# Kernel tuning notes

Measured on AMD Instinct MI355X. Metric: run time of the kernel, lower is better.

## Reference

```python
import jax, jax.numpy as jnp
import numpy as np

D_IN = 2048
D_OUT = 2048
LN_EPS = 1e-5


def setup_inputs() -> dict:
    key = jax.random.key(0)
    kx, kw, kb = jax.random.split(key, 3)
    x = jax.random.normal(kx, (8, 2048, D_IN), dtype=jnp.float32)
    # LayerNorm affine params (torch defaults: ones / zeros)
    gamma = jnp.ones((D_IN,), dtype=jnp.float32)
    beta = jnp.zeros((D_IN,), dtype=jnp.float32)
    # weight = rand(out,in)*0.001, bias = rand(out)*0.001, alpha = ones(out)
    weight = jax.random.uniform(kw, (D_OUT, D_IN), dtype=jnp.float32) * 0.001
    bias = jax.random.uniform(kb, (D_OUT,), dtype=jnp.float32) * 0.001
    alpha = jnp.ones((D_OUT,), dtype=jnp.float32)
    return {"x": x, "gamma": gamma, "beta": beta, "weight": weight,
            "bias": bias, "alpha": alpha}


def reference(x, gamma, beta, weight, bias, alpha):
    # LayerNorm over last dim (biased variance, eps=1e-5, affine)
    mu = jnp.mean(x, axis=-1, keepdims=True)
    var = jnp.mean(jnp.square(x - mu), axis=-1, keepdims=True)
    xn = (x - mu) * jax.lax.rsqrt(var + LN_EPS) * gamma + beta
    # Binarize activations: hard sign
    a = jnp.sign(xn)
    # Binarize weights: mean-center per output row, clip, sign (STE in fwd == sign)
    centered = weight - jnp.mean(weight, axis=1, keepdims=True)  # [O, I]
    signed_w = jnp.sign(centered)
    # Linear + bias, then per-output-channel alpha scale
    out = jnp.einsum('bsi,oi->bso', a, signed_w) + bias
    return out * alpha
```

## Files before the change

### kernel.cpp

```cpp
#include <hip/hip_runtime.h>

#define DIN 2048
#define WPR 64
#define QPR 32
#define GPR 16
#define RPB 8
#define LN_EPS 1e-5f

#define GLOBAL_AS __attribute__((address_space(1)))
#define LDS_AS    __attribute__((address_space(3)))

typedef unsigned long long u64;
typedef int   i32x4  __attribute__((ext_vector_type(4)));
typedef int   i32x8  __attribute__((ext_vector_type(8)));
typedef float f32x16 __attribute__((ext_vector_type(16)));

__device__ inline float wave_sum(float v) {
    #pragma unroll
    for (int off = 32; off; off >>= 1) v += __shfl_down(v, off, 64);
    return v;
}


__global__ __launch_bounds__(256) void expand_kernel(const float* __restrict__ x,
                                                     const float* __restrict__ gamma,
                                                     const float* __restrict__ beta,
                                                     const float* __restrict__ w,
                                                     char* __restrict__ Aexp,
                                                     char* __restrict__ Bexp,
                                                     int Mblocks) {
    const int t = threadIdx.x;
    const int wid = t >> 6, lane = t & 63;
    __shared__ float red[4][2 * RPB];
    __shared__ __align__(16) unsigned stg[RPB * 256];

    const bool isA = (int)blockIdx.x < Mblocks;
    const int r0 = (isA ? (int)blockIdx.x : ((int)blockIdx.x - Mblocks)) * RPB;
    const float* src = isA ? x : w;

    float gg[8], bb[8];
    if (isA) {
        float4 g0 = ((const float4*)gamma)[t * 2];
        float4 g1 = ((const float4*)gamma)[t * 2 + 1];
        float4 b0 = ((const float4*)beta)[t * 2];
        float4 b1 = ((const float4*)beta)[t * 2 + 1];
        gg[0]=g0.x; gg[1]=g0.y; gg[2]=g0.z; gg[3]=g0.w;
        gg[4]=g1.x; gg[5]=g1.y; gg[6]=g1.z; gg[7]=g1.w;
        bb[0]=b0.x; bb[1]=b0.y; bb[2]=b0.z; bb[3]=b0.w;
        bb[4]=b1.x; bb[5]=b1.y; bb[6]=b1.z; bb[7]=b1.w;
    }

    float vv[RPB][8];
    #pragma unroll
    for (int rr = 0; rr < RPB; ++rr) {
        const float* xr = src + (size_t)(r0 + rr) * DIN;
        float4 v0 = ((const float4*)xr)[t * 2];
        float4 v1 = ((const float4*)xr)[t * 2 + 1];
        vv[rr][0]=v0.x; vv[rr][1]=v0.y; vv[rr][2]=v0.z; vv[rr][3]=v0.w;
        vv[rr][4]=v1.x; vv[rr][5]=v1.y; vv[rr][6]=v1.z; vv[rr][7]=v1.w;
    }

    #pragma unroll
    for (int rr = 0; rr < RPB; ++rr) {
        float s = 0.f, ss = 0.f;
        #pragma unroll
        for (int j = 0; j < 8; ++j) s += vv[rr][j];
        if (isA) {
            #pragma unroll
            for (int j = 0; j < 8; ++j) ss += vv[rr][j] * vv[rr][j];
        }
        s = wave_sum(s);
        if (isA) ss = wave_sum(ss);
        if (lane == 0) { red[wid][rr * 2] = s; red[wid][rr * 2 + 1] = ss; }
    }
    __syncthreads();

    #pragma unroll
    for (int rr = 0; rr < RPB; ++rr) {
        float tot = red[0][rr*2] + red[1][rr*2] + red[2][rr*2] + red[3][rr*2];
        float mu  = tot * (1.f / DIN);
        unsigned word = 0;
        if (isA) {
            float tots = red[0][rr*2+1] + red[1][rr*2+1] + red[2][rr*2+1] + red[3][rr*2+1];
            float var  = tots * (1.f / DIN) - mu * mu;
            float rs   = rsqrtf(var + LN_EPS);
            #pragma unroll
            for (int j = 0; j < 8; ++j) {
                float xn = (vv[rr][j] - mu) * rs * gg[j] + bb[j];
                word |= (xn < 0.f ? 0xAu : 0x2u) << (4 * j);
            }
        } else {
            #pragma unroll
            for (int j = 0; j < 8; ++j)
                word |= ((vv[rr][j] - mu) < 0.f ? 0xAu : 0x2u) << (4 * j);
        }
        stg[rr * 256 + (((t >> 2) ^ rr) << 2) + (t & 3)] = word;
    }
    __syncthreads();

    char* dstbase = isA ? Aexp : Bexp;
    const int bm  = r0 >> 8;
    const int rt  = (r0 >> 5) & 7;
    const int ri0 = r0 & 31;
    #pragma unroll
    for (int i2 = 0; i2 < 2; ++i2) {
        const int u  = i2 * 256 + t;
        const int sc = u >> 5;
        const int kt = (u >> 4) & 1, hb = (u >> 3) & 1, ri = u & 7;
        const int g  = sc * 4 + kt * 2 + hb;
        uint4 v = *(const uint4*)&stg[ri * 256 + ((g ^ ri) << 2)];
        const size_t doff = (((size_t)(bm * 16 + sc)) * 8 + rt) * 2048 + kt * 1024 +
                            (ri0 + ri + 32 * hb) * 16;
        *(uint4*)(dstbase + doff) = v;
    }
}

__global__ __launch_bounds__(256, 3) void fp4gemm_kernel(const char* __restrict__ Aexp,
                                                         const char* __restrict__ Bexp,
                                                         const float* __restrict__ bias,
                                                         const float* __restrict__ alpha,
                                                         float* __restrict__ out,
                                                         int ldc, int nBmX) {
    const int t = threadIdx.x;
    const int wv = t >> 6, lane = t & 63;
    const int xcd = blockIdx.x & 7;
    const int loc = blockIdx.x >> 3;
    const int bm = xcd * nBmX + (loc % nBmX);
    const int bn = loc / nBmX;
    const int wr = wv >> 1, wc = wv & 1;

    const char* gA = Aexp + (size_t)(bm >> 1) * 262144 + (size_t)(bm & 1) * 8192 + lane * 16;
    const char* gB = Bexp + (size_t)(bn >> 1) * 262144 + (size_t)(bn & 1) * 8192 + lane * 16;

#define LOADF(S, AF, BF)                                                        \
    {                                                                           \
        _Pragma("unroll")                                                       \
        for (int kt = 0; kt < 2; ++kt) {                                        \
            _Pragma("unroll")                                                   \
            for (int i = 0; i < 2; ++i)                                         \
                AF[kt][i] = *(const i32x4*)(gA + (size_t)(S) * 16384 +          \
                                            (wr * 2 + i) * 2048 + kt * 1024);   \
            _Pragma("unroll")                                                   \
            for (int j = 0; j < 2; ++j)                                         \
                BF[kt][j] = *(const i32x4*)(gB + (size_t)(S) * 16384 +          \
                                            (wc * 2 + j) * 2048 + kt * 1024);   \
        }                                                                       \
    }

#define COMPF(AF, BF)                                                           \
    {                                                                           \
        _Pragma("unroll")                                                       \
        for (int kt = 0; kt < 2; ++kt) {                                        \
            i32x8 aa[2], bb2[2];                                                \
            _Pragma("unroll")                                                   \
            for (int i = 0; i < 2; ++i) {                                       \
                aa[i][0]=AF[kt][i][0]; aa[i][1]=AF[kt][i][1];                   \
                aa[i][2]=AF[kt][i][2]; aa[i][3]=AF[kt][i][3];                   \
                aa[i][4]=AF[kt][i][0]; aa[i][5]=AF[kt][i][1];                   \
                aa[i][6]=AF[kt][i][2]; aa[i][7]=AF[kt][i][3];                   \
                bb2[i][0]=BF[kt][i][0]; bb2[i][1]=BF[kt][i][1];                 \
                bb2[i][2]=BF[kt][i][2]; bb2[i][3]=BF[kt][i][3];                 \
                bb2[i][4]=BF[kt][i][0]; bb2[i][5]=BF[kt][i][1];                 \
                bb2[i][6]=BF[kt][i][2]; bb2[i][7]=BF[kt][i][3];                 \
            }                                                                   \
            __builtin_amdgcn_s_setprio(1);                                      \
            _Pragma("unroll")                                                   \
            for (int i = 0; i < 2; ++i)                                         \
                _Pragma("unroll")                                               \
                for (int j = 0; j < 2; ++j)                                     \
                    acc[i][j] = __builtin_amdgcn_mfma_scale_f32_32x32x64_f8f6f4(\
                        aa[i], bb2[j], acc[i][j], 4, 4,                         \
                        0, 0x7F7F7F7F, 0, 0x7F7F7F7F);                          \
            __builtin_amdgcn_s_setprio(0);                                      \
        }                                                                       \
    }

    f32x16 acc[2][2];
    #pragma unroll
    for (int i = 0; i < 2; ++i)
        #pragma unroll
        for (int j = 0; j < 2; ++j)
            #pragma unroll
            for (int e = 0; e < 16; ++e) acc[i][j][e] = 0.f;

    i32x4 af0[2][2], bf0[2][2], af1[2][2], bf1[2][2];

    LOADF(0, af0, bf0)
    #pragma unroll 1
    for (int s = 0; s < 14; s += 2) {
        LOADF(s + 1, af1, bf1)
        COMPF(af0, bf0)
        LOADF(s + 2, af0, bf0)
        COMPF(af1, bf1)
    }
    LOADF(15, af1, bf1)
    COMPF(af0, bf0)
    COMPF(af1, bf1)
#undef LOADF
#undef COMPF

    const int cl = lane & 31;
    const int rb = 4 * (lane >> 5);
    #pragma unroll
    for (int i = 0; i < 2; ++i) {
        #pragma unroll
        for (int j = 0; j < 2; ++j) {
            const int col = bn * 128 + wc * 64 + j * 32 + cl;
            const float bi = bias[col], al = alpha[col];
            const int row0 = bm * 128 + wr * 64 + i * 32 + rb;
            #pragma unroll
            for (int reg = 0; reg < 16; ++reg) {
                const int row = row0 + (reg & 3) + 8 * (reg >> 2);
                __builtin_nontemporal_store((acc[i][j][reg] + bi) * al,
                                            &out[(size_t)row * ldc + col]);
            }
        }
    }
}

__global__ __launch_bounds__(256) void w_pack_kernel(const float* __restrict__ w,
                                                     unsigned* __restrict__ wpk) {
    const int row = blockIdx.x;
    const int t = threadIdx.x;
    const float* wr = w + (size_t)row * DIN;
    float4 v0 = ((const float4*)wr)[t * 2];
    float4 v1 = ((const float4*)wr)[t * 2 + 1];
    float s = v0.x + v0.y + v0.z + v0.w + v1.x + v1.y + v1.z + v1.w;

    __shared__ float red[4];
    float wsum = wave_sum(s);
    int wid = t >> 6, lane = t & 63;
    if (lane == 0) red[wid] = wsum;
    __syncthreads();
    float mu = (red[0] + red[1] + red[2] + red[3]) * (1.f / DIN);

    float vv[8] = {v0.x, v0.y, v0.z, v0.w, v1.x, v1.y, v1.z, v1.w};
    unsigned byte = 0;
    #pragma unroll
    for (int j = 0; j < 8; ++j)
        byte |= ((vv[j] - mu) < 0.f ? 1u : 0u) << j;

    __shared__ unsigned char bytes[256];
    bytes[t] = (unsigned char)byte;
    __syncthreads();
    if (t < 64) {
        unsigned wd = (unsigned)bytes[t * 4] | ((unsigned)bytes[t * 4 + 1] << 8) |
                      ((unsigned)bytes[t * 4 + 2] << 16) | ((unsigned)bytes[t * 4 + 3] << 24);
        wpk[(size_t)row * WPR + t] = wd;
    }
}

__global__ __launch_bounds__(256) void ln_pack_kernel(const float* __restrict__ x,
                                                      const float* __restrict__ gamma,
                                                      const float* __restrict__ beta,
                                                      unsigned* __restrict__ apk) {
    const int row = blockIdx.x;
    const int t = threadIdx.x;
    const float* xr = x + (size_t)row * DIN;
    float4 v0 = ((const float4*)xr)[t * 2];
    float4 v1 = ((const float4*)xr)[t * 2 + 1];
    float s  = v0.x + v0.y + v0.z + v0.w + v1.x + v1.y + v1.z + v1.w;
    float ss = v0.x * v0.x + v0.y * v0.y + v0.z * v0.z + v0.w * v0.w +
               v1.x * v1.x + v1.y * v1.y + v1.z * v1.z + v1.w * v1.w;

    __shared__ float red[8];
    float wsum = wave_sum(s), wssum = wave_sum(ss);
    int wid = t >> 6, lane = t & 63;
    if (lane == 0) { red[wid] = wsum; red[4 + wid] = wssum; }
    __syncthreads();
    float tot  = red[0] + red[1] + red[2] + red[3];
    float tots = red[4] + red[5] + red[6] + red[7];
    float mu  = tot * (1.f / DIN);
    float var = tots * (1.f / DIN) - mu * mu;
    float rs  = rsqrtf(var + LN_EPS);

    float4 g0 = ((const float4*)gamma)[t * 2];
    float4 g1 = ((const float4*)gamma)[t * 2 + 1];
    float4 b0 = ((const float4*)beta)[t * 2];
    float4 b1 = ((const float4*)beta)[t * 2 + 1];
    float vv[8] = {v0.x, v0.y, v0.z, v0.w, v1.x, v1.y, v1.z, v1.w};
    float gg[8] = {g0.x, g0.y, g0.z, g0.w, g1.x, g1.y, g1.z, g1.w};
    float bb[8] = {b0.x, b0.y, b0.z, b0.w, b1.x, b1.y, b1.z, b1.w};
    unsigned byte = 0;
    #pragma unroll
    for (int j = 0; j < 8; ++j) {
        float xn = (vv[j] - mu) * rs * gg[j] + bb[j];
        byte |= (xn < 0.f ? 1u : 0u) << j;
    }

    __shared__ unsigned char bytes[256];
    bytes[t] = (unsigned char)byte;
    __syncthreads();
    if (t < 64) {
        unsigned wd = (unsigned)bytes[t * 4] | ((unsigned)bytes[t * 4 + 1] << 8) |
                      ((unsigned)bytes[t * 4 + 2] << 16) | ((unsigned)bytes[t * 4 + 3] << 24);
        apk[(size_t)row * WPR + t] = wd;
    }
}

__global__ __launch_bounds__(256) void bingemm_kernel(const u64* __restrict__ A,
                                                      const u64* __restrict__ B,
                                                      const float* __restrict__ bias,
                                                      const float* __restrict__ alpha,
                                                      float* __restrict__ out) {
    __shared__ u64 S[2 * 128 * QPR];
    uint4* Sg = (uint4*)S;
    const int t = threadIdx.x;
    const int bn = blockIdx.x, bm = blockIdx.y;

    const uint4* Ag = (const uint4*)(A + (size_t)bm * 128 * QPR);
    #pragma unroll
    for (int i = 0; i < 8; ++i) {
        int id = t + i * 256;
        int row = id >> 4, g = id & 15;
        Sg[(row << 4) + (g ^ (row & 15))] = Ag[id];
    }
    const uint4* Bg = (const uint4*)(B + (size_t)bn * 128 * QPR);
    #pragma unroll
    for (int i = 0; i < 8; ++i) {
        int id = t + i * 256;
        int row = id >> 4, g = id & 15;
        Sg[2048 + (row << 4) + (g ^ (row & 15))] = Bg[id];
    }
    __syncthreads();

    const int tr = t >> 4;
    const int tc = t & 15;
    const ulonglong2* Sq = (const ulonglong2*)S;
    const int abase = tr * GPR;
    const int bbase = 2048 + tc * GPR;

    int acc[8][8] = {};
    u64 a0[8][2], b0[8][2], a1[8][2], b1[8][2];

#define LOADK(KK, AR, BR)                                            \
    {                                                                \
        const int ka = abase + ((KK) ^ tr);                          \
        const int kb = bbase + ((KK) ^ tc);                          \
        _Pragma("unroll")                                            \
        for (int r = 0; r < 8; ++r) {                                \
            ulonglong2 v = Sq[ka + r * 256];                         \
            AR[r][0] = v.x; AR[r][1] = v.y;                          \
        }                                                            \
        _Pragma("unroll")                                            \
        for (int c2 = 0; c2 < 8; ++c2) {                             \
            ulonglong2 v = Sq[kb + c2 * 256];                        \
            BR[c2][0] = v.x; BR[c2][1] = v.y;                        \
        }                                                            \
    }

#define COMPK(AR, BR)                                                \
    {                                                                \
        _Pragma("unroll")                                            \
        for (int r = 0; r < 8; ++r) {                                \
            _Pragma("unroll")                                        \
            for (int c2 = 0; c2 < 8; ++c2) {                         \
                acc[r][c2] += __popcll(AR[r][0] ^ BR[c2][0]);        \
                acc[r][c2] += __popcll(AR[r][1] ^ BR[c2][1]);        \
            }                                                        \
        }                                                            \
    }

    LOADK(0, a0, b0);
    #pragma unroll 1
    for (int kk = 0; kk < 14; kk += 2) {
        LOADK(kk + 1, a1, b1);
        COMPK(a0, b0);
        LOADK(kk + 2, a0, b0);
        COMPK(a1, b1);
    }
    LOADK(15, a1, b1);
    COMPK(a0, b0);
    COMPK(a1, b1);
#undef LOADK
#undef COMPK

    float bi[8], al[8];
    #pragma unroll
    for (int c2 = 0; c2 < 8; ++c2) {
        int col = bn * 128 + tc + 16 * c2;
        bi[c2] = bias[col];
        al[c2] = alpha[col];
    }
    #pragma unroll
    for (int r = 0; r < 8; ++r) {
        const size_t row = (size_t)bm * 128 + tr + 16 * r;
        float* op = out + row * 2048 + bn * 128 + tc;
        #pragma unroll
        for (int c2 = 0; c2 < 8; ++c2)
            op[16 * c2] = ((float)(DIN - 2 * acc[r][c2]) + bi[c2]) * al[c2];
    }
}

extern "C" void kernel_launch(void* const* d_in, const int* in_sizes, int n_in,
                              void* d_out, int out_size, void* d_ws, size_t ws_size,
                              hipStream_t stream) {
    const float* x     = (const float*)d_in[0];
    const float* gamma = (const float*)d_in[1];
    const float* beta  = (const float*)d_in[2];
    const float* w     = (const float*)d_in[3];
    const float* bias  = (const float*)d_in[4];
    const float* alpha = (const float*)d_in[5];
    float* out = (float*)d_out;

    const int M = in_sizes[0] / DIN;
    const int N = in_sizes[3] / DIN;

    const size_t needA = (size_t)M * (DIN / 2);
    const size_t needB = (size_t)N * (DIN / 2);

    if (ws_size >= needA + needB && (M % 1024) == 0 && N == 2048) {
        char* Aexp = (char*)d_ws;
        char* Bexp = (char*)d_ws + needA;
        expand_kernel<<<(M + N) / RPB, 256, 0, stream>>>(x, gamma, beta, w,
                                                         Aexp, Bexp, M / RPB);
        const int nBmX = (M / 128) / 8;
        dim3 grid((M / 128) * (N / 128));
        fp4gemm_kernel<<<grid, 256, 0, stream>>>(Aexp, Bexp, bias, alpha, out,
                                                 N, nBmX);
    } else {
        unsigned* apk = (unsigned*)d_ws;
        unsigned* wpk = (unsigned*)((char*)d_ws + (size_t)M * WPR * 4);
        w_pack_kernel<<<N, 256, 0, stream>>>(w, wpk);
        ln_pack_kernel<<<M, 256, 0, stream>>>(x, gamma, beta, apk);
        dim3 grid(N / 128, M / 128);
        bingemm_kernel<<<grid, 256, 0, stream>>>((const u64*)apk, (const u64*)wpk,
                                                 bias, alpha, out);
    }
}
```

Measured before the change: 86.06 us.

## Stage shared A fragments through triple-buffered LDS with async global-to-LDS loads

Instead of every wave loading its A fragments straight from global memory, the block now stages each A k-slice once into a triple-buffered LDS array using global_load_lds. Waves that share the same A rows read from LDS, while B fragments are still register-double-buffered from global. The aim is to remove the duplicated A global and L2 traffic between the two waves that share rows, and to prefetch two stages ahead. In exchange it adds 24KB of LDS, a block barrier with manual vmcnt waits on every k-step, and runtime conditionals inside the loop.

New measurement: 83.89 us. -2.5%, faster.

```diff
diff --git a/kernel.cpp b/kernel.cpp
--- a/kernel.cpp
+++ b/kernel.cpp
@@ -121,6 +121,7 @@
                                                          const float* __restrict__ alpha,
                                                          float* __restrict__ out,
                                                          int ldc, int nBmX) {
+    __shared__ char As[3][8192];
     const int t = threadIdx.x;
     const int wv = t >> 6, lane = t & 63;
     const int xcd = blockIdx.x & 7;
@@ -129,39 +130,52 @@
     const int bn = loc / nBmX;
     const int wr = wv >> 1, wc = wv & 1;
 
-    const char* gA = Aexp + (size_t)(bm >> 1) * 262144 + (size_t)(bm & 1) * 8192 + lane * 16;
+    const char* gA = Aexp + (size_t)(bm >> 1) * 262144 + (size_t)(bm & 1) * 8192;
     const char* gB = Bexp + (size_t)(bn >> 1) * 262144 + (size_t)(bn & 1) * 8192 + lane * 16;
 
-#define LOADF(S, AF, BF)                                                        \
+#define STAGE(BUF, S)                                                           \
     {                                                                           \
         _Pragma("unroll")                                                       \
-        for (int kt = 0; kt < 2; ++kt) {                                        \
-            _Pragma("unroll")                                                   \
-            for (int i = 0; i < 2; ++i)                                         \
-                AF[kt][i] = *(const i32x4*)(gA + (size_t)(S) * 16384 +          \
-                                            (wr * 2 + i) * 2048 + kt * 1024);   \
+        for (int i2 = 0; i2 < 2; ++i2) {                                        \
+            const int ch = wv * 2 + i2;                                         \
+            __builtin_amdgcn_global_load_lds(                                   \
+                (const GLOBAL_AS unsigned*)(gA + (size_t)(S) * 16384 + ch * 1024 + lane * 16), \
+                (LDS_AS unsigned*)(&As[BUF][ch * 1024]), 16, 0, 0);             \
+        }                                                                       \
+    }
+
+#define LOADB(S, BF)                                                            \
+    {                                                                           \
+        _Pragma("unroll")                                                       \
+        for (int kt = 0; kt < 2; ++kt)                                          \
             _Pragma("unroll")                                                   \
             for (int j = 0; j < 2; ++j)                                         \
                 BF[kt][j] = *(const i32x4*)(gB + (size_t)(S) * 16384 +          \
                                             (wc * 2 + j) * 2048 + kt * 1024);   \
+    }
+
+#define STEP(S, BFUSE, BFLOAD)                                                  \
+    {                                                                           \
+        if ((S) <= 14) LOADB((S) + 1, BFLOAD)                                   \
+        if ((S) <= 13) {                                                        \
+            const int nb = (c == 0) ? 2 : c - 1;                                \
+            STAGE(nb, (S) + 2)                                                  \
         }                                                                       \
-    }
-
-#define COMPF(AF, BF)                                                           \
-    {                                                                           \
         _Pragma("unroll")                                                       \
         for (int kt = 0; kt < 2; ++kt) {                                        \
+            i32x4 a[2];                                                         \
+            _Pragma("unroll")                                                   \
+            for (int i = 0; i < 2; ++i)                                         \
+                a[i] = *(const i32x4*)&As[c][(wr * 2 + i) * 2048 + kt * 1024 + lane * 16]; \
             i32x8 aa[2], bb2[2];                                                \
             _Pragma("unroll")                                                   \
             for (int i = 0; i < 2; ++i) {                                       \
-                aa[i][0]=AF[kt][i][0]; aa[i][1]=AF[kt][i][1];                   \
-                aa[i][2]=AF[kt][i][2]; aa[i][3]=AF[kt][i][3];                   \
-                aa[i][4]=AF[kt][i][0]; aa[i][5]=AF[kt][i][1];                   \
-                aa[i][6]=AF[kt][i][2]; aa[i][7]=AF[kt][i][3];                   \
-                bb2[i][0]=BF[kt][i][0]; bb2[i][1]=BF[kt][i][1];                 \
-                bb2[i][2]=BF[kt][i][2]; bb2[i][3]=BF[kt][i][3];                 \
-                bb2[i][4]=BF[kt][i][0]; bb2[i][5]=BF[kt][i][1];                 \
-                bb2[i][6]=BF[kt][i][2]; bb2[i][7]=BF[kt][i][3];                 \
+                aa[i][0]=a[i][0]; aa[i][1]=a[i][1]; aa[i][2]=a[i][2]; aa[i][3]=a[i][3]; \
+                aa[i][4]=a[i][0]; aa[i][5]=a[i][1]; aa[i][6]=a[i][2]; aa[i][7]=a[i][3]; \
+                bb2[i][0]=BFUSE[kt][i][0]; bb2[i][1]=BFUSE[kt][i][1];           \
+                bb2[i][2]=BFUSE[kt][i][2]; bb2[i][3]=BFUSE[kt][i][3];           \
+                bb2[i][4]=BFUSE[kt][i][0]; bb2[i][5]=BFUSE[kt][i][1];           \
+                bb2[i][6]=BFUSE[kt][i][2]; bb2[i][7]=BFUSE[kt][i][3];           \
             }                                                                   \
             __builtin_amdgcn_s_setprio(1);                                      \
             _Pragma("unroll")                                                   \
@@ -173,6 +187,13 @@
                         0, 0x7F7F7F7F, 0, 0x7F7F7F7F);                          \
             __builtin_amdgcn_s_setprio(0);                                      \
         }                                                                       \
+        if ((S) < 15) {                                                         \
+            if ((S) <= 13) { asm volatile("s_waitcnt vmcnt(2)" ::: "memory"); } \
+            else           { asm volatile("s_waitcnt vmcnt(0)" ::: "memory"); } \
+            __builtin_amdgcn_s_barrier();                                       \
+            asm volatile("" ::: "memory");                                      \
+            c = (c == 2) ? 0 : c + 1;                                           \
+        }                                                                       \
     }
 
     f32x16 acc[2][2];
@@ -183,21 +204,24 @@
             #pragma unroll
             for (int e = 0; e < 16; ++e) acc[i][j][e] = 0.f;
 
-    i32x4 af0[2][2], bf0[2][2], af1[2][2], bf1[2][2];
-
-    LOADF(0, af0, bf0)
+    i32x4 bfA[2][2], bfB[2][2];
+
+    STAGE(0, 0)
+    LOADB(0, bfA)
+    STAGE(1, 1)
+    asm volatile("s_waitcnt vmcnt(2)" ::: "memory");
+    __builtin_amdgcn_s_barrier();
+    asm volatile("" ::: "memory");
+
+    int c = 0;
     #pragma unroll 1
-    for (int s = 0; s < 14; s += 2) {
-        LOADF(s + 1, af1, bf1)
-        COMPF(af0, bf0)
-        LOADF(s + 2, af0, bf0)
-        COMPF(af1, bf1)
-    }
-    LOADF(15, af1, bf1)
-    COMPF(af0, bf0)
-    COMPF(af1, bf1)
-#undef LOADF
-#undef COMPF
+    for (int s = 0; s < 16; s += 2) {
+        STEP(s,     bfA, bfB)
+        STEP(s + 1, bfB, bfA)
+    }
+#undef STEP
+#undef LOADB
+#undef STAGE
 
     const int cl = lane & 31;
     const int rb = 4 * (lane >> 5);
```
